# Optimization experiments

Measured on AMD Instinct MI355X. Metric: run time of the kernel, lower is better.

## Reference

```python
import jax, jax.numpy as jnp
import numpy as np

B, T, K, DIM = 32, 12, 16, 512
H0, H1 = 512, 256


def setup_inputs() -> dict:
    key = jax.random.key(0)
    k0, k1, k2, k3, k4 = jax.random.split(key, 5)
    return {
        "sets_of_objects": jax.random.normal(k0, (B, T, K, DIM), dtype=jnp.float32),
        "W0": jax.random.normal(k1, (2 * DIM, H0), dtype=jnp.float32) * 0.02,
        "b0": jnp.zeros((H0,), dtype=jnp.float32),
        "W1": jax.random.normal(k2, (H0, H1), dtype=jnp.float32) * 0.02,
        "b1": jnp.zeros((H1,), dtype=jnp.float32),
        "D": DIM,
    }


def reference(sets_of_objects, W0, b0, W1, b1, D):
    Bb, Tt, Kk, Dm = sets_of_objects.shape
    Tm1 = Tt - 1
    # Eval path: for each t in 1..T-1, original code builds all-pairs concat of
    # O_t with itself (O_1 is unused in create_inter_object_cat), runs the MLP,
    # then avg-pools over t identical copies (no-op on e) and clamps the summed mask.
    O_t = sets_of_objects[:, 1:]                                   # [B, T-1, K, D]
    A = jnp.broadcast_to(O_t[:, :, :, None, :], (Bb, Tm1, Kk, Kk, Dm))   # first obj k repeated
    Bo = jnp.broadcast_to(O_t[:, :, None, :, :], (Bb, Tm1, Kk, Kk, Dm))  # second obj j
    pairs = jnp.concatenate([A, Bo], axis=-1).reshape(Bb, Tm1, Kk * Kk, 2 * Dm)
    # EncoderMLP: Linear -> ReLU per hidden layer
    h = jax.nn.relu(pairs @ W0 + b0)                               # [B, T-1, K*K, H0]
    e = jax.nn.relu(h @ W1 + b1)                                   # [B, T-1, K*K, H1]
    # object-presence masks (clamp of feature sums)
    is_first = jnp.clip(pairs[..., :D].sum(-1), 0.0, 1.0)          # [B, T-1, K*K]
    is_second = jnp.clip(pairs[..., D:].sum(-1), 0.0, 1.0)
    # clamp(sum over t identical copies, 0, 1) == clamp(t * v, 0, 1)
    counts = jnp.arange(1, Tt, dtype=e.dtype)[None, :, None]
    is_obj = jnp.clip(counts * is_first * is_second, 0.0, 1.0)
    return e, is_obj
```

## Files before the change

### kernel.cpp

```cpp
#include <hip/hip_runtime.h>
#include <hip/hip_bf16.h>

#define B_    32
#define T_    12
#define TM1   11
#define K_    16
#define DIM_  512
#define H0_   512
#define H1_   256
#define NROWS 5632
#define NBT   352
#define E_ELEMS (NBT*256*H1_)

typedef __bf16 bf16x8 __attribute__((ext_vector_type(8)));
typedef float  f32x16 __attribute__((ext_vector_type(16)));
typedef unsigned u32x4 __attribute__((ext_vector_type(4)));

#define OFRAG_OFF   0
#define W0FRAG_OFF  5767168
#define W1FRAG_OFF  (W0FRAG_OFF + 1048576)
#define UB_OFF      (W1FRAG_OFF + 262144)
#define VSW_OFF     (UB_OFF + 5767168)

__device__ __forceinline__ unsigned bf_rn(float f) {
    unsigned u = __float_as_uint(f);
    return (u + 0x7fffu + ((u >> 16) & 1u)) >> 16;
}
__device__ __forceinline__ unsigned pk_bf16(float lo, float hi) {
    return bf_rn(lo) | (bf_rn(hi) << 16);
}
__device__ __forceinline__ unsigned short f2bf(float f) {
    return (unsigned short)bf_rn(f);
}
__device__ __forceinline__ float bfu_lo(unsigned u) { return __uint_as_float(u << 16); }
__device__ __forceinline__ float bfu_hi(unsigned u) { return __uint_as_float(u & 0xffff0000u); }
__device__ __forceinline__ unsigned cvt_pk(float lo, float hi) {
    unsigned r;
    asm("v_cvt_pk_bf16_f32 %0, %1, %2" : "=v"(r) : "v"(lo), "v"(hi));
    return r;
}

__global__ __launch_bounds__(256) void k_prep(const float* __restrict__ W0,
                                              const float* __restrict__ W1,
                                              const float* __restrict__ O,
                                              char* __restrict__ ws)
{
    const int unit = blockIdx.x * 4 + (threadIdx.x >> 6);
    const int l = threadIdx.x & 63;
    if (unit < 1280) {
        const float* src; size_t dstoff; int stride;
        if (unit < 1024) {
            int half = unit >> 9, s = (unit >> 4) & 31, nt = unit & 15;
            int k = s*16 + (l >> 5)*8;
            int n = nt*32 + (l & 31);
            src = W0 + (size_t)(half*512 + k) * H0_ + n;
            stride = H0_;
            dstoff = W0FRAG_OFF + (((size_t)(half*32 + s)*16 + nt)*64 + l)*16;
        } else {
            int r = unit - 1024; int s = r >> 3, ct = r & 7;
            int k = s*16 + (l >> 5)*8;
            int n = ct*32 + (l & 31);
            src = W1 + (size_t)k * H1_ + n;
            stride = H1_;
            dstoff = W1FRAG_OFF + (((size_t)(s*8 + ct))*64 + l)*16;
        }
        float f[8];
        #pragma unroll
        for (int j = 0; j < 8; ++j) f[j] = src[(size_t)j * stride];
        u32x4 o = { pk_bf16(f[0],f[1]), pk_bf16(f[2],f[3]), pk_bf16(f[4],f[5]), pk_bf16(f[6],f[7]) };
        *(u32x4*)(ws + dstoff) = o;
    } else {
        const int u = unit - 1280;
        const int s = u / 176, mt = u % 176;
        const int row = mt*32 + (l & 31);
        const int b  = row / (TM1*K_);
        const int rem = row % (TM1*K_);
        const int t  = rem / K_;
        const int i  = rem % K_;
        const float* src = O + (((size_t)(b*T_ + t + 1)*K_ + i)*DIM_) + s*16 + (l >> 5)*8;
        float4 a = *(const float4*)src;
        float4 c = *(const float4*)(src + 4);
        u32x4 o = { pk_bf16(a.x,a.y), pk_bf16(a.z,a.w), pk_bf16(c.x,c.y), pk_bf16(c.z,c.w) };
        *(u32x4*)(ws + OFRAG_OFF + ((size_t)(s*176 + mt)*64 + l)*16) = o;
    }
}

__global__ __launch_bounds__(256) void k_uv(char* __restrict__ ws,
                                            const float* __restrict__ b0)
{
    const int mb = blockIdx.x;
    const int t  = threadIdx.x, l = t & 63;
    const int nb = blockIdx.y * 4 + (t >> 6);
    const int half = nb >> 3;
    const char* Ag = ws + OFRAG_OFF + ((size_t)(mb*2)*64 + l)*16;
    const char* Bg = ws + W0FRAG_OFF + (size_t)half*524288 + ((size_t)((nb&7)*2)*64 + l)*16;
    const size_t AS = 176*1024, BS = 16*1024;

    f32x16 acc[2][2];
    #pragma unroll
    for (int p = 0; p < 2; ++p)
        #pragma unroll
        for (int c = 0; c < 2; ++c)
            #pragma unroll
            for (int r = 0; r < 16; ++r) acc[p][c][r] = 0.f;

    u32x4 aA[2], bA[2], aB[2], bB[2];
    #pragma unroll
    for (int p = 0; p < 2; ++p) {
        aA[p] = *(const u32x4*)(Ag + 0*AS + p*1024);
        bA[p] = *(const u32x4*)(Bg + 0*BS + p*1024);
        aB[p] = *(const u32x4*)(Ag + 1*AS + p*1024);
        bB[p] = *(const u32x4*)(Bg + 1*BS + p*1024);
    }

    for (int ss = 0; ss < 32; ss += 2) {
        {
            union { u32x4 u[2]; bf16x8 b[2]; } af, bf;
            af.u[0]=aA[0]; af.u[1]=aA[1]; bf.u[0]=bA[0]; bf.u[1]=bA[1];
            if (ss + 2 < 32) {
                #pragma unroll
                for (int p = 0; p < 2; ++p) {
                    aA[p] = *(const u32x4*)(Ag + (size_t)(ss+2)*AS + p*1024);
                    bA[p] = *(const u32x4*)(Bg + (size_t)(ss+2)*BS + p*1024);
                }
            }
            acc[0][0] = __builtin_amdgcn_mfma_f32_32x32x16_bf16(af.b[0], bf.b[0], acc[0][0], 0,0,0);
            acc[0][1] = __builtin_amdgcn_mfma_f32_32x32x16_bf16(af.b[0], bf.b[1], acc[0][1], 0,0,0);
            acc[1][0] = __builtin_amdgcn_mfma_f32_32x32x16_bf16(af.b[1], bf.b[0], acc[1][0], 0,0,0);
            acc[1][1] = __builtin_amdgcn_mfma_f32_32x32x16_bf16(af.b[1], bf.b[1], acc[1][1], 0,0,0);
        }
        {
            union { u32x4 u[2]; bf16x8 b[2]; } af, bf;
            af.u[0]=aB[0]; af.u[1]=aB[1]; bf.u[0]=bB[0]; bf.u[1]=bB[1];
            if (ss + 3 < 32) {
                #pragma unroll
                for (int p = 0; p < 2; ++p) {
                    aB[p] = *(const u32x4*)(Ag + (size_t)(ss+3)*AS + p*1024);
                    bB[p] = *(const u32x4*)(Bg + (size_t)(ss+3)*BS + p*1024);
                }
            }
            acc[0][0] = __builtin_amdgcn_mfma_f32_32x32x16_bf16(af.b[0], bf.b[0], acc[0][0], 0,0,0);
            acc[0][1] = __builtin_amdgcn_mfma_f32_32x32x16_bf16(af.b[0], bf.b[1], acc[0][1], 0,0,0);
            acc[1][0] = __builtin_amdgcn_mfma_f32_32x32x16_bf16(af.b[1], bf.b[0], acc[1][0], 0,0,0);
            acc[1][1] = __builtin_amdgcn_mfma_f32_32x32x16_bf16(af.b[1], bf.b[1], acc[1][1], 0,0,0);
        }
    }

    #pragma unroll
    for (int p = 0; p < 2; ++p) {
        #pragma unroll
        for (int c = 0; c < 2; ++c) {
            const int col = (nb & 7)*64 + c*32 + (l & 31);
            const float bias = (half == 0) ? b0[col] : 0.f;
            #pragma unroll
            for (int r = 0; r < 16; ++r) {
                const int row = (r & 3) + 8*(r >> 2) + 4*(l >> 5);
                const int M = mb*64 + p*32 + row;
                const float v = acc[p][c][r] + bias;
                if (half == 0) {
                    *(unsigned short*)(ws + UB_OFF + ((size_t)M*512 + col)*2) = f2bf(v);
                } else {
                    const int bt = M >> 4, j = M & 15;
                    const int cc = col >> 3;
                    const int c2 = ((cc ^ (j & 7)) << 3) | (col & 7);
                    *(unsigned short*)(ws + VSW_OFF + ((size_t)(bt*16 + j)*512 + c2)*2) = f2bf(v);
                }
            }
        }
    }
}

__global__ __launch_bounds__(256) void k_obj(const float* __restrict__ O,
                                             float* __restrict__ out)
{
    __shared__ float red[16][16];
    __shared__ float fl[16];
    const int bt = blockIdx.x;
    const int b_ = bt / TM1, tt = bt % TM1;
    const int t  = threadIdx.x;
    const int i  = t >> 4, s = t & 15;
    const float* base = O + (((size_t)(b_ * T_ + tt + 1) * K_ + i) * DIM_) + s * 32;
    float sum = 0.f;
    #pragma unroll
    for (int q = 0; q < 8; ++q) {
        float4 v = *(const float4*)(base + q * 4);
        sum += v.x + v.y + v.z + v.w;
    }
    red[i][s] = sum;
    __syncthreads();
    if (t < 16) {
        float f = 0.f;
        #pragma unroll
        for (int s2 = 0; s2 < 16; ++s2) f += red[t][s2];
        fl[t] = fminf(fmaxf(f, 0.f), 1.f);
    }
    __syncthreads();
    const float val = fminf((float)(tt + 1) * fl[t >> 4] * fl[t & 15], 1.f);
    __builtin_nontemporal_store(val, out + (size_t)E_ELEMS + (size_t)bt * 256 + t);
}

#define EBODY(S, WUSE, WLD, DOLOAD)                                            \
    do {                                                                       \
        if (DOLOAD) {                                                          \
            _Pragma("unroll")                                                  \
            for (int c_ = 0; c_ < 4; ++c_)                                     \
                WLD[c_] = *(const u32x4*)(Wg + (size_t)((S)+2)*8192 + c_*1024);\
        }                                                                      \
        const int vchunk_ = ((S)*2 + kc) ^ (jj & 7);                           \
        u32x4 vu_ = *(const u32x4*)(Vs + jj*1024 + vchunk_*16);                \
        float vf_[8];                                                          \
        _Pragma("unroll")                                                      \
        for (int q_ = 0; q_ < 4; ++q_) {                                       \
            vf_[2*q_] = bfu_lo(vu_[q_]); vf_[2*q_+1] = bfu_hi(vu_[q_]);        \
        }                                                                      \
        bf16x8 afrag_[2];                                                      \
        _Pragma("unroll")                                                      \
        for (int p_ = 0; p_ < 2; ++p_) {                                       \
            const int iloc_ = wp*4 + p_*2 + ih;                                \
            u32x4 uu_ = *(const u32x4*)(Us + iloc_*1024 + (S)*32 + kc*16);     \
            u32x4 o_;                                                          \
            _Pragma("unroll")                                                  \
            for (int q_ = 0; q_ < 4; ++q_) {                                   \
                float h0_ = fmaxf(bfu_lo(uu_[q_]) + vf_[2*q_],   0.f);         \
                float h1_ = fmaxf(bfu_hi(uu_[q_]) + vf_[2*q_+1], 0.f);         \
                o_[q_] = cvt_pk(h0_, h1_);                                     \
            }                                                                  \
            union { u32x4 u; bf16x8 b; } cv_; cv_.u = o_; afrag_[p_] = cv_.b;  \
        }                                                                      \
        union { u32x4 u[4]; bf16x8 b[4]; } wcu_;                               \
        _Pragma("unroll")                                                      \
        for (int c_ = 0; c_ < 4; ++c_) wcu_.u[c_] = WUSE[c_];                  \
        _Pragma("unroll")                                                      \
        for (int p_ = 0; p_ < 2; ++p_)                                         \
            _Pragma("unroll")                                                  \
            for (int c_ = 0; c_ < 4; ++c_)                                     \
                acc[p_][c_] = __builtin_amdgcn_mfma_f32_32x32x16_bf16(         \
                    afrag_[p_], wcu_.b[c_], acc[p_][c_], 0, 0, 0);             \
    } while (0)

__global__ __launch_bounds__(256, 2) void k_e(const char* __restrict__ ws,
                                              const float* __restrict__ b1,
                                              float* __restrict__ out)
{
    __shared__ alignas(16) char lds[24576];
    char* Us = lds;
    char* Vs = lds + 8192;

    const int bid = blockIdx.x;
    const int bt = bid >> 1, ph = bid & 1;
    const int t = threadIdx.x, l = t & 63, w = t >> 6;
    const int wp = w & 1, wc = w >> 1;

    const char* Ug = ws + UB_OFF  + (size_t)(bt*16 + ph*8) * 1024;
    const char* Vg = ws + VSW_OFF + (size_t)bt * 16384;
    const char* Wg = ws + W1FRAG_OFF + (size_t)(wc*4)*1024 + (size_t)l*16;

    #pragma unroll
    for (int r = 0; r < 2; ++r) { int c = t + r*256; *(u32x4*)(Us + c*16) = *(const u32x4*)(Ug + c*16); }
    #pragma unroll
    for (int r = 0; r < 4; ++r) { int c = t + r*256; *(u32x4*)(Vs + c*16) = *(const u32x4*)(Vg + c*16); }
    __syncthreads();

    f32x16 acc[2][4];
    #pragma unroll
    for (int p = 0; p < 2; ++p)
        #pragma unroll
        for (int c = 0; c < 4; ++c)
            #pragma unroll
            for (int r = 0; r < 16; ++r) acc[p][c][r] = 0.f;

    const int jj = l & 15;
    const int kc = l >> 5;
    const int ih = (l >> 4) & 1;

    u32x4 wk0[4], wk1[4], wk2[4], wk3[4];
    #pragma unroll
    for (int c = 0; c < 4; ++c) wk0[c] = *(const u32x4*)(Wg + c*1024);
    #pragma unroll
    for (int c = 0; c < 4; ++c) wk1[c] = *(const u32x4*)(Wg + 8192 + c*1024);

    for (int j = 0; j < 8; ++j) {
        const int s = j * 4;
        EBODY(s+0, wk0, wk2, true);
        EBODY(s+1, wk1, wk3, true);
        EBODY(s+2, wk2, wk0, (j < 7));
        EBODY(s+3, wk3, wk1, (j < 7));
    }

    #pragma unroll
    for (int c = 0; c < 4; ++c) {
        const int col = wc*128 + c*32 + (l & 31);
        const float bb = b1[col];
        #pragma unroll
        for (int p = 0; p < 2; ++p) {
            #pragma unroll
            for (int r = 0; r < 16; ++r) {
                const int pair = ph*128 + wp*64 + p*32 + (r & 3) + 8*(r >> 2) + 4*(l >> 5);
                const float v = fmaxf(acc[p][c][r] + bb, 0.f);
                __builtin_nontemporal_store(v, out + ((size_t)bt*256 + pair)*256 + col);
            }
        }
    }
}

extern "C" void kernel_launch(void* const* d_in, const int* in_sizes, int n_in,
                              void* d_out, int out_size, void* d_ws, size_t ws_size,
                              hipStream_t stream) {
    const float* O  = (const float*)d_in[0];
    const float* W0 = (const float*)d_in[1];
    const float* b0 = (const float*)d_in[2];
    const float* W1 = (const float*)d_in[3];
    const float* b1 = (const float*)d_in[4];
    float* out = (float*)d_out;
    char* ws = (char*)d_ws;

    k_prep<<<1728, 256, 0, stream>>>(W0, W1, O, ws);
    dim3 guv(88, 4);
    k_uv<<<guv, 256, 0, stream>>>(ws, b0);
    k_obj<<<NBT, 256, 0, stream>>>(O, out);
    k_e<<<NBT * 2, 256, 0, stream>>>(ws, b1, out);
}
```

Baseline: 67.85 us.

## Split k_e work across more blocks with smaller per-wave tiles for occupancy

The second-layer kernel now launches four blocks per (b,t) instead of two. Each block covers one half of the output columns and each wave computes a single 32-row tile instead of two, which halves the accumulator registers. Weight prefetch is simplified to double buffering, and launch bounds are raised to allow three blocks per CU. The aim is more waves in flight to hide latency, at the cost of each block reloading the U/V tiles into LDS and less reuse of every W1 fragment across rows.

```diff
diff --git a/kernel.cpp b/kernel.cpp
--- a/kernel.cpp
+++ b/kernel.cpp
@@ -14,6 +14,7 @@
 
 typedef __bf16 bf16x8 __attribute__((ext_vector_type(8)));
 typedef float  f32x16 __attribute__((ext_vector_type(16)));
+typedef float  f32x4  __attribute__((ext_vector_type(4)));
 typedef unsigned u32x4 __attribute__((ext_vector_type(4)));
 
 #define OFRAG_OFF   0
@@ -199,46 +200,29 @@
     __builtin_nontemporal_store(val, out + (size_t)E_ELEMS + (size_t)bt * 256 + t);
 }
 
-#define EBODY(S, WUSE, WLD, DOLOAD)                                            \
+#define KSTEP(S, WK)                                                           \
     do {                                                                       \
-        if (DOLOAD) {                                                          \
-            _Pragma("unroll")                                                  \
-            for (int c_ = 0; c_ < 4; ++c_)                                     \
-                WLD[c_] = *(const u32x4*)(Wg + (size_t)((S)+2)*8192 + c_*1024);\
-        }                                                                      \
-        const int vchunk_ = ((S)*2 + kc) ^ (jj & 7);                           \
-        u32x4 vu_ = *(const u32x4*)(Vs + jj*1024 + vchunk_*16);                \
-        float vf_[8];                                                          \
+        const int vch_ = (((S)*2 + kc) ^ jlow_);                               \
+        u32x4 vu_ = *(const u32x4*)(VsL + vch_*16);                            \
+        u32x4 uu_ = *(const u32x4*)(UsL + (S)*32);                             \
+        u32x4 o_;                                                              \
         _Pragma("unroll")                                                      \
         for (int q_ = 0; q_ < 4; ++q_) {                                       \
-            vf_[2*q_] = bfu_lo(vu_[q_]); vf_[2*q_+1] = bfu_hi(vu_[q_]);        \
+            float h0_ = fmaxf(bfu_lo(uu_[q_]) + bfu_lo(vu_[q_]), 0.f);         \
+            float h1_ = fmaxf(bfu_hi(uu_[q_]) + bfu_hi(vu_[q_]), 0.f);         \
+            o_[q_] = cvt_pk(h0_, h1_);                                         \
         }                                                                      \
-        bf16x8 afrag_[2];                                                      \
+        union { u32x4 u; bf16x8 b; } af_; af_.u = o_;                          \
+        union { u32x4 u[4]; bf16x8 b[4]; } wu_;                                \
         _Pragma("unroll")                                                      \
-        for (int p_ = 0; p_ < 2; ++p_) {                                       \
-            const int iloc_ = wp*4 + p_*2 + ih;                                \
-            u32x4 uu_ = *(const u32x4*)(Us + iloc_*1024 + (S)*32 + kc*16);     \
-            u32x4 o_;                                                          \
-            _Pragma("unroll")                                                  \
-            for (int q_ = 0; q_ < 4; ++q_) {                                   \
-                float h0_ = fmaxf(bfu_lo(uu_[q_]) + vf_[2*q_],   0.f);         \
-                float h1_ = fmaxf(bfu_hi(uu_[q_]) + vf_[2*q_+1], 0.f);         \
-                o_[q_] = cvt_pk(h0_, h1_);                                     \
-            }                                                                  \
-            union { u32x4 u; bf16x8 b; } cv_; cv_.u = o_; afrag_[p_] = cv_.b;  \
-        }                                                                      \
-        union { u32x4 u[4]; bf16x8 b[4]; } wcu_;                               \
-        _Pragma("unroll")                                                      \
-        for (int c_ = 0; c_ < 4; ++c_) wcu_.u[c_] = WUSE[c_];                  \
-        _Pragma("unroll")                                                      \
-        for (int p_ = 0; p_ < 2; ++p_)                                         \
-            _Pragma("unroll")                                                  \
-            for (int c_ = 0; c_ < 4; ++c_)                                     \
-                acc[p_][c_] = __builtin_amdgcn_mfma_f32_32x32x16_bf16(         \
-                    afrag_[p_], wcu_.b[c_], acc[p_][c_], 0, 0, 0);             \
+        for (int c_ = 0; c_ < 4; ++c_) wu_.u[c_] = WK[c_];                     \
+        acc0 = __builtin_amdgcn_mfma_f32_32x32x16_bf16(af_.b, wu_.b[0], acc0, 0,0,0); \
+        acc1 = __builtin_amdgcn_mfma_f32_32x32x16_bf16(af_.b, wu_.b[1], acc1, 0,0,0); \
+        acc2 = __builtin_amdgcn_mfma_f32_32x32x16_bf16(af_.b, wu_.b[2], acc2, 0,0,0); \
+        acc3 = __builtin_amdgcn_mfma_f32_32x32x16_bf16(af_.b, wu_.b[3], acc3, 0,0,0); \
     } while (0)
 
-__global__ __launch_bounds__(256, 2) void k_e(const char* __restrict__ ws,
+__global__ __launch_bounds__(256, 3) void k_e(const char* __restrict__ ws,
                                               const float* __restrict__ b1,
                                               float* __restrict__ out)
 {
@@ -247,13 +231,12 @@
     char* Vs = lds + 8192;
 
     const int bid = blockIdx.x;
-    const int bt = bid >> 1, ph = bid & 1;
-    const int t = threadIdx.x, l = t & 63, w = t >> 6;
-    const int wp = w & 1, wc = w >> 1;
+    const int ch = bid & 1, ph = (bid >> 1) & 1, bt = bid >> 2;
+    const int t = threadIdx.x, l = t & 63, wp = t >> 6;
 
     const char* Ug = ws + UB_OFF  + (size_t)(bt*16 + ph*8) * 1024;
     const char* Vg = ws + VSW_OFF + (size_t)bt * 16384;
-    const char* Wg = ws + W1FRAG_OFF + (size_t)(wc*4)*1024 + (size_t)l*16;
+    const char* Wg = ws + W1FRAG_OFF + (size_t)(ch*4)*1024 + (size_t)l*16;
 
     #pragma unroll
     for (int r = 0; r < 2; ++r) { int c = t + r*256; *(u32x4*)(Us + c*16) = *(const u32x4*)(Ug + c*16); }
@@ -261,46 +244,53 @@
     for (int r = 0; r < 4; ++r) { int c = t + r*256; *(u32x4*)(Vs + c*16) = *(const u32x4*)(Vg + c*16); }
     __syncthreads();
 
-    f32x16 acc[2][4];
-    #pragma unroll
-    for (int p = 0; p < 2; ++p)
+    f32x16 acc0, acc1, acc2, acc3;
+    #pragma unroll
+    for (int r = 0; r < 16; ++r) { acc0[r] = 0.f; acc1[r] = 0.f; acc2[r] = 0.f; acc3[r] = 0.f; }
+
+    const int jj   = l & 15;
+    const int jlow_ = jj & 7;
+    const int kc   = l >> 5;
+    const int il   = wp*2 + ((l >> 4) & 1);
+    const char* UsL = Us + il*1024 + kc*16;
+    const char* VsL = Vs + jj*1024;
+
+    u32x4 wA[4], wB[4];
+    #pragma unroll
+    for (int c = 0; c < 4; ++c) wA[c] = *(const u32x4*)(Wg + c*1024);
+
+    for (int sj = 0; sj < 16; ++sj) {
+        const int s0 = sj * 2;
         #pragma unroll
         for (int c = 0; c < 4; ++c)
+            wB[c] = *(const u32x4*)(Wg + (size_t)(s0+1)*8192 + c*1024);
+        KSTEP(s0, wA);
+        if (sj < 15) {
             #pragma unroll
-            for (int r = 0; r < 16; ++r) acc[p][c][r] = 0.f;
-
-    const int jj = l & 15;
-    const int kc = l >> 5;
-    const int ih = (l >> 4) & 1;
-
-    u32x4 wk0[4], wk1[4], wk2[4], wk3[4];
-    #pragma unroll
-    for (int c = 0; c < 4; ++c) wk0[c] = *(const u32x4*)(Wg + c*1024);
-    #pragma unroll
-    for (int c = 0; c < 4; ++c) wk1[c] = *(const u32x4*)(Wg + 8192 + c*1024);
-
-    for (int j = 0; j < 8; ++j) {
-        const int s = j * 4;
-        EBODY(s+0, wk0, wk2, true);
-        EBODY(s+1, wk1, wk3, true);
-        EBODY(s+2, wk2, wk0, (j < 7));
-        EBODY(s+3, wk3, wk1, (j < 7));
-    }
-
-    #pragma unroll
-    for (int c = 0; c < 4; ++c) {
-        const int col = wc*128 + c*32 + (l & 31);
-        const float bb = b1[col];
-        #pragma unroll
-        for (int p = 0; p < 2; ++p) {
-            #pragma unroll
-            for (int r = 0; r < 16; ++r) {
-                const int pair = ph*128 + wp*64 + p*32 + (r & 3) + 8*(r >> 2) + 4*(l >> 5);
-                const float v = fmaxf(acc[p][c][r] + bb, 0.f);
-                __builtin_nontemporal_store(v, out + ((size_t)bt*256 + pair)*256 + col);
-            }
-        }
-    }
+            for (int c = 0; c < 4; ++c)
+                wA[c] = *(const u32x4*)(Wg + (size_t)(s0+2)*8192 + c*1024);
+        }
+        KSTEP(s0+1, wB);
+    }
+
+    const int colb = ch*128 + (l & 31);
+    const int pr0  = ph*128 + wp*32 + 4*(l >> 5);
+    float* ob = out + ((size_t)bt*256 + pr0)*256 + colb;
+    #define EPI(ACC, CT)                                                       \
+        do {                                                                   \
+            const float bb_ = b1[colb + (CT)*32];                              \
+            _Pragma("unroll")                                                  \
+            for (int r_ = 0; r_ < 16; ++r_) {                                  \
+                const int rr_ = (r_ & 3) + 8*(r_ >> 2);                        \
+                __builtin_nontemporal_store(fmaxf(ACC[r_] + bb_, 0.f),         \
+                    ob + (size_t)rr_*256 + (CT)*32);                           \
+            }                                                                  \
+        } while (0)
+    EPI(acc0, 0);
+    EPI(acc1, 1);
+    EPI(acc2, 2);
+    EPI(acc3, 3);
+    #undef EPI
 }
 
 extern "C" void kernel_launch(void* const* d_in, const int* in_sizes, int n_in,
@@ -318,5 +308,5 @@
     dim3 guv(88, 4);
     k_uv<<<guv, 256, 0, stream>>>(ws, b0);
     k_obj<<<NBT, 256, 0, stream>>>(O, out);
-    k_e<<<NBT * 2, 256, 0, stream>>>(ws, b1, out);
-}
+    k_e<<<NBT * 4, 256, 0, stream>>>(ws, b1, out);
+}
```

Measured after the change: 70.10 us. 1.03x slower.
